# Performance work log

Measured on AMD Instinct MI355X. Metric: run time of the kernel, lower is better.

Reference implementation:

```python
import jax, jax.numpy as jnp
import numpy as np

N, T, U, D, V = 16, 512, 64, 512, 500


def _ragged_indices(enc_len, dec_len):
    """Flat (b, t, u) index triples for all valid T_i x U_i pairs, concatenated."""
    bs, ts, us = [], [], []
    for i in range(len(enc_len)):
        t, u = int(enc_len[i]), int(dec_len[i])
        tt, uu = np.meshgrid(np.arange(t), np.arange(u), indexing='ij')
        bs.append(np.full(t * u, i, dtype=np.int32))
        ts.append(tt.ravel().astype(np.int32))
        us.append(uu.ravel().astype(np.int32))
    return (jnp.asarray(np.concatenate(bs)),
            jnp.asarray(np.concatenate(ts)),
            jnp.asarray(np.concatenate(us)))


def setup_inputs() -> dict:
    key = jax.random.key(0)
    k1, k2, k3, k4 = jax.random.split(key, 4)
    encoder_out = jax.random.normal(k1, (N, T, D), dtype=jnp.float32)
    decoder_out = jax.random.normal(k2, (N, U, D), dtype=jnp.float32)
    # Concrete (non-traced) ragged lengths, as in the torch module's .tolist().
    rng = np.random.default_rng(0)
    enc_len = rng.integers(T // 2, T + 1, size=N)
    dec_len = rng.integers(U // 2, U + 1, size=N)
    b_idx, t_idx, u_idx = _ragged_indices(enc_len, dec_len)
    # nn.Linear(D, V) parameters
    bound = 1.0 / np.sqrt(D)
    W = jax.random.uniform(k3, (V, D), minval=-bound, maxval=bound, dtype=jnp.float32)
    b = jax.random.uniform(k4, (V,), minval=-bound, maxval=bound, dtype=jnp.float32)
    return {
        'encoder_out': encoder_out,
        'decoder_out': decoder_out,
        'W': W,
        'b': b,
        'b_idx': b_idx,
        't_idx': t_idx,
        'u_idx': u_idx,
    }


def reference(encoder_out, decoder_out, W, b, b_idx, t_idx, u_idx):
    # Ragged broadcast add: x[k] = encoder_out[b_k, t_k] + decoder_out[b_k, u_k]
    x = encoder_out[b_idx, t_idx] + decoder_out[b_idx, u_idx]  # (sum_TU, D)
    activations = jnp.tanh(x)
    logits = activations @ W.T + b  # (sum_TU, V)
    return logits
```

## Files before the change

kernel.cpp:

```cpp
#include <hip/hip_runtime.h>
#include <hip/hip_bf16.h>


typedef __attribute__((ext_vector_type(4))) int   i32x4;
typedef __attribute__((ext_vector_type(4))) float f32x4;
typedef __attribute__((ext_vector_type(8))) short short8;

__device__ __forceinline__ unsigned short f2bf(float v) {
    unsigned int u = __float_as_uint(v);
    u += 0x7fffu + ((u >> 16) & 1u);
    return (unsigned short)(u >> 16);
}

__device__ __forceinline__ unsigned pack_bf16x2(float a, float b) {
    __hip_bfloat162 h = __float22bfloat162_rn(make_float2(a, b));
    unsigned u;
    __builtin_memcpy(&u, &h, 4);
    return u;
}

__device__ __forceinline__ float bflo(unsigned u) { return __uint_as_float(u << 16); }
__device__ __forceinline__ float bfhi(unsigned u) { return __uint_as_float(u & 0xffff0000u); }

__device__ __forceinline__ float tanh_fast(float x) {
    float t = __builtin_amdgcn_exp2f(x * 2.8853900817779268f);
    return (t - 1.0f) * __builtin_amdgcn_rcpf(t + 1.0f);
}

__device__ __forceinline__ unsigned q8(float t) {
    return __float_as_uint(fmaf(t, 127.0f, 12582912.0f)) & 0xffu;
}

__global__ void prep_cast_kernel(const float* __restrict__ src,
                                 unsigned short* __restrict__ dst, int n4) {
    const int i = blockIdx.x * blockDim.x + threadIdx.x;
    if (i < n4) {
        const float4 v = reinterpret_cast<const float4*>(src)[i];
        uint2 p;
        p.x = pack_bf16x2(v.x, v.y);
        p.y = pack_bf16x2(v.z, v.w);
        reinterpret_cast<uint2*>(dst)[i] = p;
    }
}

__global__ void prep_wq_kernel(const float* __restrict__ W,
                               signed char* __restrict__ qW, float* __restrict__ fac) {
    const int n   = blockIdx.x;
    const int tid = threadIdx.x;
    float w = 0.0f;
    if (n < 500) w = W[n * 512 + tid];
    float m = fabsf(w);
    #pragma unroll
    for (int off = 32; off; off >>= 1) m = fmaxf(m, __shfl_xor(m, off));
    __shared__ float wm[8];
    if ((tid & 63) == 0) wm[tid >> 6] = m;
    __syncthreads();
    const float mx = fmaxf(fmaxf(fmaxf(wm[0], wm[1]), fmaxf(wm[2], wm[3])),
                           fmaxf(fmaxf(wm[4], wm[5]), fmaxf(wm[6], wm[7])));
    const float inv = (mx > 0.0f) ? 127.0f / mx : 0.0f;
    qW[n * 512 + tid] = (signed char)(int)rintf(w * inv);
    if (tid == 0) fac[n] = mx * (1.0f / (127.0f * 127.0f));
}

template<bool BF16G>
__global__ __launch_bounds__(512, 4)
void joiner_i8_kernel(const float* __restrict__ enc, const float* __restrict__ dec,
                      const unsigned short* __restrict__ encB,
                      const unsigned short* __restrict__ decB,
                      const float* __restrict__ bias,
                      const signed char* __restrict__ qW, const float* __restrict__ fac,
                      const int* __restrict__ b_idx, const int* __restrict__ t_idx,
                      const int* __restrict__ u_idx,
                      float* __restrict__ out, int M)
{
    __shared__ unsigned char Abuf[65792];

    const int tid  = threadIdx.x;
    const int lane = tid & 63;
    const int m0   = blockIdx.x * 64;

    const int rr = tid >> 7;
    int eoff_l, doff_l;
    {
        const int rc = min(m0 + ((lane & 15) << 2) + rr, M - 1);
        const int bi = b_idx[rc];
        eoff_l = ((bi << 9) + t_idx[rc]) << 9;
        doff_l = ((bi << 6) + u_idx[rc]) << 9;
    }

    {
        const int kq  = tid & 127;
        const int kq4 = kq << 2;

        if constexpr (BF16G) {
            uint2 es[6], dsv[6];
            #pragma unroll
            for (int i = 0; i < 6; ++i) {
                const int eo = __builtin_amdgcn_readlane(eoff_l, i);
                const int dofs = __builtin_amdgcn_readlane(doff_l, i);
                es[i]  = *reinterpret_cast<const uint2*>(encB + eo + kq4);
                dsv[i] = *reinterpret_cast<const uint2*>(decB + dofs + kq4);
            }
            #pragma unroll
            for (int p = 0; p < 16; ++p) {
                const int s = p % 6;
                const uint2 e = es[s];
                const uint2 d = dsv[s];
                if (p + 6 < 16) {
                    const int eo = __builtin_amdgcn_readlane(eoff_l, p + 6);
                    const int dofs = __builtin_amdgcn_readlane(doff_l, p + 6);
                    es[s]  = *reinterpret_cast<const uint2*>(encB + eo + kq4);
                    dsv[s] = *reinterpret_cast<const uint2*>(decB + dofs + kq4);
                }
                const unsigned u = q8(tanh_fast(bflo(e.x) + bflo(d.x)))
                                 | (q8(tanh_fast(bfhi(e.x) + bfhi(d.x))) << 8)
                                 | (q8(tanh_fast(bflo(e.y) + bflo(d.y))) << 16)
                                 | (q8(tanh_fast(bfhi(e.y) + bfhi(d.y))) << 24);
                const int r = p * 4 + rr;
                const int byteoff = (r * 512) + ((kq * 4) ^ ((r & 7) << 4));
                *reinterpret_cast<unsigned*>(&Abuf[byteoff]) = u;
            }
        } else {
            float4 es[6], dsv[6];
            #pragma unroll
            for (int i = 0; i < 6; ++i) {
                const int eo = __builtin_amdgcn_readlane(eoff_l, i);
                const int dofs = __builtin_amdgcn_readlane(doff_l, i);
                es[i]  = *reinterpret_cast<const float4*>(enc + eo + kq4);
                dsv[i] = *reinterpret_cast<const float4*>(dec + dofs + kq4);
            }
            #pragma unroll
            for (int p = 0; p < 16; ++p) {
                const int s = p % 6;
                const float4 e = es[s];
                const float4 d = dsv[s];
                if (p + 6 < 16) {
                    const int eo = __builtin_amdgcn_readlane(eoff_l, p + 6);
                    const int dofs = __builtin_amdgcn_readlane(doff_l, p + 6);
                    es[s]  = *reinterpret_cast<const float4*>(enc + eo + kq4);
                    dsv[s] = *reinterpret_cast<const float4*>(dec + dofs + kq4);
                }
                const unsigned u = q8(tanh_fast(e.x + d.x))
                                 | (q8(tanh_fast(e.y + d.y)) << 8)
                                 | (q8(tanh_fast(e.z + d.z)) << 16)
                                 | (q8(tanh_fast(e.w + d.w)) << 24);
                const int r = p * 4 + rr;
                const int byteoff = (r * 512) + ((kq * 4) ^ ((r & 7) << 4));
                *reinterpret_cast<unsigned*>(&Abuf[byteoff]) = u;
            }
        }
    }

    const int wv   = tid >> 6;
    const int l15  = lane & 15;
    const int lk   = lane >> 4;
    const int n_wave = wv << 6;
    const int a_swz  = (l15 & 7) << 4;

    i32x4 acc[4][4];
    #pragma unroll
    for (int mf = 0; mf < 4; ++mf)
        #pragma unroll
        for (int nf = 0; nf < 4; ++nf)
            acc[mf][nf] = (i32x4)(0);

    const signed char* wq = qW + ((size_t)(n_wave + l15)) * 512 + lk * 16;
    auto loadB = [&](int ks, int nf) -> i32x4 {
        return *reinterpret_cast<const i32x4*>(wq + nf * (16 * 512) + ks * 64);
    };

    i32x4 Bf[2][4];
    #pragma unroll
    for (int nf = 0; nf < 4; ++nf) Bf[0][nf] = loadB(0, nf);
    #pragma unroll
    for (int nf = 0; nf < 4; ++nf) Bf[1][nf] = loadB(1, nf);

    __syncthreads();

    #pragma unroll
    for (int ks = 0; ks < 8; ++ks) {
        i32x4 a[4];
        #pragma unroll
        for (int mf = 0; mf < 4; ++mf) {
            const int addr = ((mf * 16 + l15) << 9) + ((ks * 64 + lk * 16) ^ a_swz);
            a[mf] = *reinterpret_cast<const i32x4*>(&Abuf[addr]);
        }
        __builtin_amdgcn_s_setprio(1);
        #pragma unroll
        for (int mf = 0; mf < 4; ++mf)
            #pragma unroll
            for (int nf = 0; nf < 4; ++nf)
                acc[mf][nf] = __builtin_amdgcn_mfma_i32_16x16x64_i8(a[mf], Bf[ks & 1][nf], acc[mf][nf], 0, 0, 0);
        __builtin_amdgcn_s_setprio(0);
        if (ks < 6) {
            #pragma unroll
            for (int nf = 0; nf < 4; ++nf) Bf[ks & 1][nf] = loadB(ks + 2, nf);
        }
    }

    float accf[4][4][4];
    #pragma unroll
    for (int nf = 0; nf < 4; ++nf) {
        const int col = n_wave + nf * 16 + l15;
        const float fc = (col < 500) ? fac[col] : 0.0f;
        const float bv = (col < 500) ? bias[col] : 0.0f;
        #pragma unroll
        for (int mf = 0; mf < 4; ++mf)
            #pragma unroll
            for (int j = 0; j < 4; ++j)
                accf[mf][nf][j] = (float)acc[mf][nf][j] * fc + bv;
    }

    float* Obuf = reinterpret_cast<float*>(Abuf);
    #pragma unroll
    for (int h = 0; h < 2; ++h) {
        __syncthreads();
        if ((wv >> 2) == h) {
            const int lcol = (wv & 3) << 6;
            #pragma unroll
            for (int mf = 0; mf < 4; ++mf)
                #pragma unroll
                for (int nf = 0; nf < 4; ++nf)
                    #pragma unroll
                    for (int j = 0; j < 4; ++j) {
                        const int r = mf * 16 + lk * 4 + j;
                        Obuf[r * 257 + lcol + nf * 16 + l15] = accf[mf][nf][j];
                    }
        }
        __syncthreads();
        #pragma unroll
        for (int i = 0; i < 8; ++i) {
            const int linear = i * 512 + tid;
            const int r  = linear >> 6;
            const int c4 = linear & 63;
            const int row = m0 + r;
            const int col = (h << 8) + (c4 << 2);
            if (row < M && col < 500) {
                const f32x4 v = *reinterpret_cast<const f32x4*>(&Obuf[r * 257 + (c4 << 2)]);
                __builtin_nontemporal_store(v, reinterpret_cast<f32x4*>(&out[(size_t)row * 500 + col]));
            }
        }
    }
}

__global__ __launch_bounds__(512, 4)
void joiner_fallback_kernel(const float* __restrict__ enc, const float* __restrict__ dec,
                            const float* __restrict__ W, const float* __restrict__ bias,
                            const int* __restrict__ b_idx, const int* __restrict__ t_idx,
                            const int* __restrict__ u_idx,
                            float* __restrict__ out, int M)
{
    __shared__ unsigned char Abuf[65792];
    const int tid  = threadIdx.x;
    const int lane = tid & 63;
    const int m0   = blockIdx.x * 64;

    const int rr = tid >> 7;
    int eoff_l, doff_l;
    {
        const int rc = min(m0 + ((lane & 15) << 2) + rr, M - 1);
        const int bi = b_idx[rc];
        eoff_l = ((bi << 9) + t_idx[rc]) << 9;
        doff_l = ((bi << 6) + u_idx[rc]) << 9;
    }
    {
        const int kq  = tid & 127;
        const int kq4 = kq << 2;
        float4 es[6], dsv[6];
        #pragma unroll
        for (int i = 0; i < 6; ++i) {
            es[i]  = *reinterpret_cast<const float4*>(enc + __builtin_amdgcn_readlane(eoff_l, i) + kq4);
            dsv[i] = *reinterpret_cast<const float4*>(dec + __builtin_amdgcn_readlane(doff_l, i) + kq4);
        }
        #pragma unroll
        for (int p = 0; p < 16; ++p) {
            const int s = p % 6;
            const float4 e = es[s];
            const float4 d = dsv[s];
            if (p + 6 < 16) {
                es[s]  = *reinterpret_cast<const float4*>(enc + __builtin_amdgcn_readlane(eoff_l, p + 6) + kq4);
                dsv[s] = *reinterpret_cast<const float4*>(dec + __builtin_amdgcn_readlane(doff_l, p + 6) + kq4);
            }
            uint2 packed;
            packed.x = pack_bf16x2(tanh_fast(e.x + d.x), tanh_fast(e.y + d.y));
            packed.y = pack_bf16x2(tanh_fast(e.z + d.z), tanh_fast(e.w + d.w));
            const int r = p * 4 + rr;
            const int byteoff = (r * 1024 + kq * 8) ^ ((r & 7) << 4);
            *reinterpret_cast<uint2*>(&Abuf[byteoff]) = packed;
        }
    }
    const int wv   = tid >> 6;
    const int l15  = lane & 15;
    const int lk   = lane >> 4;
    const int n_wave = wv << 6;
    const int a_swz  = (l15 & 7) << 4;

    f32x4 acc[4][4];
    #pragma unroll
    for (int mf = 0; mf < 4; ++mf)
        #pragma unroll
        for (int nf = 0; nf < 4; ++nf)
            acc[mf][nf] = (f32x4)(0.0f);

    const float* wpf = W + (((size_t)(n_wave + l15)) << 9) + (lk << 3);
    const int colbase = n_wave + l15;
    auto loadB = [&](int ks, int nf) -> short8 {
        short8 b;
        float4 w0 = make_float4(0,0,0,0), w1 = make_float4(0,0,0,0);
        if (colbase + nf * 16 < 500) {
            const float4* q = reinterpret_cast<const float4*>(wpf + nf * 8192 + ks * 32);
            w0 = q[0]; w1 = q[1];
        }
        b[0] = (short)f2bf(w0.x); b[1] = (short)f2bf(w0.y);
        b[2] = (short)f2bf(w0.z); b[3] = (short)f2bf(w0.w);
        b[4] = (short)f2bf(w1.x); b[5] = (short)f2bf(w1.y);
        b[6] = (short)f2bf(w1.z); b[7] = (short)f2bf(w1.w);
        return b;
    };

    short8 Bf[2][4];
    #pragma unroll
    for (int nf = 0; nf < 4; ++nf) Bf[0][nf] = loadB(0, nf);
    #pragma unroll
    for (int nf = 0; nf < 4; ++nf) Bf[1][nf] = loadB(1, nf);
    __syncthreads();
    #pragma unroll
    for (int ks = 0; ks < 16; ++ks) {
        short8 a[4];
        #pragma unroll
        for (int mf = 0; mf < 4; ++mf) {
            const int addr = (((mf * 16 + l15) << 10) + ks * 64 + lk * 16) ^ a_swz;
            a[mf] = *reinterpret_cast<const short8*>(&Abuf[addr]);
        }
        #pragma unroll
        for (int mf = 0; mf < 4; ++mf)
            #pragma unroll
            for (int nf = 0; nf < 4; ++nf)
                acc[mf][nf] = __builtin_amdgcn_mfma_f32_16x16x32_bf16(a[mf], Bf[ks & 1][nf], acc[mf][nf], 0, 0, 0);
        if (ks < 14) {
            #pragma unroll
            for (int nf = 0; nf < 4; ++nf) Bf[ks & 1][nf] = loadB(ks + 2, nf);
        }
    }
    #pragma unroll
    for (int nf = 0; nf < 4; ++nf) {
        const int col = n_wave + nf * 16 + l15;
        const float bv = (col < 500) ? bias[col] : 0.0f;
        #pragma unroll
        for (int mf = 0; mf < 4; ++mf)
            #pragma unroll
            for (int j = 0; j < 4; ++j)
                acc[mf][nf][j] += bv;
    }
    float* Obuf = reinterpret_cast<float*>(Abuf);
    #pragma unroll
    for (int h = 0; h < 2; ++h) {
        __syncthreads();
        if ((wv >> 2) == h) {
            const int lcol = (wv & 3) << 6;
            #pragma unroll
            for (int mf = 0; mf < 4; ++mf)
                #pragma unroll
                for (int nf = 0; nf < 4; ++nf)
                    #pragma unroll
                    for (int j = 0; j < 4; ++j) {
                        const int r = mf * 16 + lk * 4 + j;
                        Obuf[r * 257 + lcol + nf * 16 + l15] = acc[mf][nf][j];
                    }
        }
        __syncthreads();
        #pragma unroll
        for (int i = 0; i < 8; ++i) {
            const int linear = i * 512 + tid;
            const int r  = linear >> 6;
            const int c4 = linear & 63;
            const int row = m0 + r;
            const int col = (h << 8) + (c4 << 2);
            if (row < M && col < 500) {
                const f32x4 v = *reinterpret_cast<const f32x4*>(&Obuf[r * 257 + (c4 << 2)]);
                __builtin_nontemporal_store(v, reinterpret_cast<f32x4*>(&out[(size_t)row * 500 + col]));
            }
        }
    }
}

extern "C" void kernel_launch(void* const* d_in, const int* in_sizes, int n_in,
                              void* d_out, int out_size, void* d_ws, size_t ws_size,
                              hipStream_t stream) {
    const float* enc  = (const float*)d_in[0];
    const float* dec  = (const float*)d_in[1];
    const float* W    = (const float*)d_in[2];
    const float* bias = (const float*)d_in[3];
    const int* bi = (const int*)d_in[4];
    const int* ti = (const int*)d_in[5];
    const int* ui = (const int*)d_in[6];
    float* out = (float*)d_out;

    const int M = in_sizes[4];
    const int grid = (M + 63) / 64;

    const int enc_n  = in_sizes[0];
    const int dec_n  = in_sizes[1];
    const size_t qw_bytes = (size_t)512 * 512;
    const size_t fac_off  = qw_bytes;
    const size_t enc_off  = fac_off + 2048;
    const size_t dec_off  = enc_off + (size_t)enc_n * 2;
    const size_t need_i8  = fac_off + 2048;
    const size_t need_all = dec_off + (size_t)dec_n * 2;

    if (ws_size >= need_all) {
        signed char* qW = (signed char*)d_ws;
        float* fac = (float*)((char*)d_ws + fac_off);
        unsigned short* encB = (unsigned short*)((char*)d_ws + enc_off);
        unsigned short* decB = (unsigned short*)((char*)d_ws + dec_off);
        prep_wq_kernel<<<512, 512, 0, stream>>>(W, qW, fac);
        prep_cast_kernel<<<(enc_n / 4 + 255) / 256, 256, 0, stream>>>(enc, encB, enc_n / 4);
        prep_cast_kernel<<<(dec_n / 4 + 255) / 256, 256, 0, stream>>>(dec, decB, dec_n / 4);
        joiner_i8_kernel<true><<<grid, 512, 0, stream>>>(
            enc, dec, encB, decB, bias, qW, fac, bi, ti, ui, out, M);
    } else if (ws_size >= need_i8) {
        signed char* qW = (signed char*)d_ws;
        float* fac = (float*)((char*)d_ws + fac_off);
        prep_wq_kernel<<<512, 512, 0, stream>>>(W, qW, fac);
        joiner_i8_kernel<false><<<grid, 512, 0, stream>>>(
            enc, dec, nullptr, nullptr, bias, qW, fac, bi, ti, ui, out, M);
    } else {
        joiner_fallback_kernel<<<grid, 512, 0, stream>>>(
            enc, dec, W, bias, bi, ti, ui, out, M);
    }
}
```

Before: 239.2 us.

## Split A-tile gather into K halves and overlap second half with MFMA

Adds a new bf16-input joiner kernel that gathers and quantizes only the first half of K into shared memory before the matmul starts. The second half's global loads are issued early and consumed inside the first half's MFMA loop, and B fragments are double-buffered from global. The aim is to hide gather and tanh latency behind tensor-core work instead of doing all of it serially up front. The cost is more registers and an extra barrier, which may reduce occupancy. The old template is reduced to its fp32 variant for the fallback path.

```diff
diff --git a/kernel.cpp b/kernel.cpp
--- a/kernel.cpp
+++ b/kernel.cpp
@@ -62,11 +62,170 @@
     if (tid == 0) fac[n] = mx * (1.0f / (127.0f * 127.0f));
 }
 
-template<bool BF16G>
+__global__ __launch_bounds__(512, 4)
+void joiner_i8p_kernel(const unsigned short* __restrict__ encB,
+                       const unsigned short* __restrict__ decB,
+                       const float* __restrict__ bias,
+                       const signed char* __restrict__ qW, const float* __restrict__ fac,
+                       const int* __restrict__ b_idx, const int* __restrict__ t_idx,
+                       const int* __restrict__ u_idx,
+                       float* __restrict__ out, int M)
+{
+    __shared__ unsigned char Abuf[65792];
+
+    const int tid  = threadIdx.x;
+    const int lane = tid & 63;
+    const int wv   = tid >> 6;
+    const int m0   = blockIdx.x * 64;
+
+    int eoff_l, doff_l;
+    {
+        const int rc = min(m0 + ((lane & 7) << 3) + wv, M - 1);
+        const int bi = b_idx[rc];
+        eoff_l = ((bi << 9) + t_idx[rc]) << 9;
+        doff_l = ((bi << 6) + u_idx[rc]) << 9;
+    }
+
+    auto gload = [&](int p, int h, uint2& e, uint2& d) {
+        const int eo   = __builtin_amdgcn_readlane(eoff_l, p) + h * 256 + lane * 4;
+        const int dofs = __builtin_amdgcn_readlane(doff_l, p) + h * 256 + lane * 4;
+        e = *reinterpret_cast<const uint2*>(encB + eo);
+        d = *reinterpret_cast<const uint2*>(decB + dofs);
+    };
+    auto gconsume = [&](int p, int h, uint2 e, uint2 d) {
+        const unsigned u = q8(tanh_fast(bflo(e.x) + bflo(d.x)))
+                         | (q8(tanh_fast(bfhi(e.x) + bfhi(d.x))) << 8)
+                         | (q8(tanh_fast(bflo(e.y) + bflo(d.y))) << 16)
+                         | (q8(tanh_fast(bfhi(e.y) + bfhi(d.y))) << 24);
+        const int r = p * 8 + wv;
+        const int byteoff = h * 16384 + r * 256 + ((lane * 4) ^ ((r & 7) << 4));
+        *reinterpret_cast<unsigned*>(&Abuf[byteoff]) = u;
+    };
+
+    const int l15  = lane & 15;
+    const int lk   = lane >> 4;
+    const int n_wave = wv << 6;
+    const int a_swz  = (l15 & 7) << 4;
+
+    const signed char* wq = qW + ((size_t)(n_wave + l15)) * 512 + lk * 16;
+    auto loadB = [&](int ks, int nf) -> i32x4 {
+        return *reinterpret_cast<const i32x4*>(wq + nf * (16 * 512) + ks * 64);
+    };
+
+    uint2 ge[8], gd[8];
+    #pragma unroll
+    for (int p = 0; p < 8; ++p) gload(p, 0, ge[p], gd[p]);
+    #pragma unroll
+    for (int p = 0; p < 8; ++p) gconsume(p, 0, ge[p], gd[p]);
+    #pragma unroll
+    for (int p = 0; p < 8; ++p) gload(p, 1, ge[p], gd[p]);
+
+    i32x4 acc[4][4];
+    #pragma unroll
+    for (int mf = 0; mf < 4; ++mf)
+        #pragma unroll
+        for (int nf = 0; nf < 4; ++nf)
+            acc[mf][nf] = (i32x4)(0);
+
+    i32x4 Bf[2][4];
+    #pragma unroll
+    for (int nf = 0; nf < 4; ++nf) Bf[0][nf] = loadB(0, nf);
+    #pragma unroll
+    for (int nf = 0; nf < 4; ++nf) Bf[1][nf] = loadB(1, nf);
+
+    __syncthreads();
+
+    #pragma unroll
+    for (int ks = 0; ks < 4; ++ks) {
+        gconsume(2 * ks,     1, ge[2 * ks],     gd[2 * ks]);
+        gconsume(2 * ks + 1, 1, ge[2 * ks + 1], gd[2 * ks + 1]);
+        i32x4 a[4];
+        #pragma unroll
+        for (int mf = 0; mf < 4; ++mf) {
+            const int addr = (mf * 16 + l15) * 256 + ((ks * 64 + lk * 16) ^ a_swz);
+            a[mf] = *reinterpret_cast<const i32x4*>(&Abuf[addr]);
+        }
+        __builtin_amdgcn_s_setprio(1);
+        #pragma unroll
+        for (int mf = 0; mf < 4; ++mf)
+            #pragma unroll
+            for (int nf = 0; nf < 4; ++nf)
+                acc[mf][nf] = __builtin_amdgcn_mfma_i32_16x16x64_i8(a[mf], Bf[ks & 1][nf], acc[mf][nf], 0, 0, 0);
+        __builtin_amdgcn_s_setprio(0);
+        #pragma unroll
+        for (int nf = 0; nf < 4; ++nf) Bf[ks & 1][nf] = loadB(ks + 2, nf);
+    }
+
+    __syncthreads();
+
+    #pragma unroll
+    for (int ks = 4; ks < 8; ++ks) {
+        i32x4 a[4];
+        #pragma unroll
+        for (int mf = 0; mf < 4; ++mf) {
+            const int addr = 16384 + (mf * 16 + l15) * 256 + (((ks - 4) * 64 + lk * 16) ^ a_swz);
+            a[mf] = *reinterpret_cast<const i32x4*>(&Abuf[addr]);
+        }
+        __builtin_amdgcn_s_setprio(1);
+        #pragma unroll
+        for (int mf = 0; mf < 4; ++mf)
+            #pragma unroll
+            for (int nf = 0; nf < 4; ++nf)
+                acc[mf][nf] = __builtin_amdgcn_mfma_i32_16x16x64_i8(a[mf], Bf[ks & 1][nf], acc[mf][nf], 0, 0, 0);
+        __builtin_amdgcn_s_setprio(0);
+        if (ks < 6) {
+            #pragma unroll
+            for (int nf = 0; nf < 4; ++nf) Bf[ks & 1][nf] = loadB(ks + 2, nf);
+        }
+    }
+
+    float accf[4][4][4];
+    #pragma unroll
+    for (int nf = 0; nf < 4; ++nf) {
+        const int col = n_wave + nf * 16 + l15;
+        const float fc = (col < 500) ? fac[col] : 0.0f;
+        const float bv = (col < 500) ? bias[col] : 0.0f;
+        #pragma unroll
+        for (int mf = 0; mf < 4; ++mf)
+            #pragma unroll
+            for (int j = 0; j < 4; ++j)
+                accf[mf][nf][j] = (float)acc[mf][nf][j] * fc + bv;
+    }
+
+    float* Obuf = reinterpret_cast<float*>(Abuf);
+    #pragma unroll
+    for (int h = 0; h < 2; ++h) {
+        __syncthreads();
+        if ((wv >> 2) == h) {
+            const int lcol = (wv & 3) << 6;
+            #pragma unroll
+            for (int mf = 0; mf < 4; ++mf)
+                #pragma unroll
+                for (int nf = 0; nf < 4; ++nf)
+                    #pragma unroll
+                    for (int j = 0; j < 4; ++j) {
+                        const int r = mf * 16 + lk * 4 + j;
+                        Obuf[r * 257 + lcol + nf * 16 + l15] = accf[mf][nf][j];
+                    }
+        }
+        __syncthreads();
+        #pragma unroll
+        for (int i = 0; i < 8; ++i) {
+            const int linear = i * 512 + tid;
+            const int r  = linear >> 6;
+            const int c4 = linear & 63;
+            const int row = m0 + r;
+            const int col = (h << 8) + (c4 << 2);
+            if (row < M && col < 500) {
+                const f32x4 v = *reinterpret_cast<const f32x4*>(&Obuf[r * 257 + (c4 << 2)]);
+                __builtin_nontemporal_store(v, reinterpret_cast<f32x4*>(&out[(size_t)row * 500 + col]));
+            }
+        }
+    }
+}
+
 __global__ __launch_bounds__(512, 4)
 void joiner_i8_kernel(const float* __restrict__ enc, const float* __restrict__ dec,
-                      const unsigned short* __restrict__ encB,
-                      const unsigned short* __restrict__ decB,
                       const float* __restrict__ bias,
                       const signed char* __restrict__ qW, const float* __restrict__ fac,
                       const int* __restrict__ b_idx, const int* __restrict__ t_idx,
@@ -74,7 +233,6 @@
                       float* __restrict__ out, int M)
 {
     __shared__ unsigned char Abuf[65792];
-
     const int tid  = threadIdx.x;
     const int lane = tid & 63;
     const int m0   = blockIdx.x * 64;
@@ -87,70 +245,33 @@
         eoff_l = ((bi << 9) + t_idx[rc]) << 9;
         doff_l = ((bi << 6) + u_idx[rc]) << 9;
     }
-
     {
         const int kq  = tid & 127;
         const int kq4 = kq << 2;
-
-        if constexpr (BF16G) {
-            uint2 es[6], dsv[6];
-            #pragma unroll
-            for (int i = 0; i < 6; ++i) {
-                const int eo = __builtin_amdgcn_readlane(eoff_l, i);
-                const int dofs = __builtin_amdgcn_readlane(doff_l, i);
-                es[i]  = *reinterpret_cast<const uint2*>(encB + eo + kq4);
-                dsv[i] = *reinterpret_cast<const uint2*>(decB + dofs + kq4);
+        float4 es[6], dsv[6];
+        #pragma unroll
+        for (int i = 0; i < 6; ++i) {
+            es[i]  = *reinterpret_cast<const float4*>(enc + __builtin_amdgcn_readlane(eoff_l, i) + kq4);
+            dsv[i] = *reinterpret_cast<const float4*>(dec + __builtin_amdgcn_readlane(doff_l, i) + kq4);
+        }
+        #pragma unroll
+        for (int p = 0; p < 16; ++p) {
+            const int s = p % 6;
+            const float4 e = es[s];
+            const float4 d = dsv[s];
+            if (p + 6 < 16) {
+                es[s]  = *reinterpret_cast<const float4*>(enc + __builtin_amdgcn_readlane(eoff_l, p + 6) + kq4);
+                dsv[s] = *reinterpret_cast<const float4*>(dec + __builtin_amdgcn_readlane(doff_l, p + 6) + kq4);
             }
-            #pragma unroll
-            for (int p = 0; p < 16; ++p) {
-                const int s = p % 6;
-                const uint2 e = es[s];
-                const uint2 d = dsv[s];
-                if (p + 6 < 16) {
-                    const int eo = __builtin_amdgcn_readlane(eoff_l, p + 6);
-                    const int dofs = __builtin_amdgcn_readlane(doff_l, p + 6);
-                    es[s]  = *reinterpret_cast<const uint2*>(encB + eo + kq4);
-                    dsv[s] = *reinterpret_cast<const uint2*>(decB + dofs + kq4);
-                }
-                const unsigned u = q8(tanh_fast(bflo(e.x) + bflo(d.x)))
-                                 | (q8(tanh_fast(bfhi(e.x) + bfhi(d.x))) << 8)
-                                 | (q8(tanh_fast(bflo(e.y) + bflo(d.y))) << 16)
-                                 | (q8(tanh_fast(bfhi(e.y) + bfhi(d.y))) << 24);
-                const int r = p * 4 + rr;
-                const int byteoff = (r * 512) + ((kq * 4) ^ ((r & 7) << 4));
-                *reinterpret_cast<unsigned*>(&Abuf[byteoff]) = u;
-            }
-        } else {
-            float4 es[6], dsv[6];
-            #pragma unroll
-            for (int i = 0; i < 6; ++i) {
-                const int eo = __builtin_amdgcn_readlane(eoff_l, i);
-                const int dofs = __builtin_amdgcn_readlane(doff_l, i);
-                es[i]  = *reinterpret_cast<const float4*>(enc + eo + kq4);
-                dsv[i] = *reinterpret_cast<const float4*>(dec + dofs + kq4);
-            }
-            #pragma unroll
-            for (int p = 0; p < 16; ++p) {
-                const int s = p % 6;
-                const float4 e = es[s];
-                const float4 d = dsv[s];
-                if (p + 6 < 16) {
-                    const int eo = __builtin_amdgcn_readlane(eoff_l, p + 6);
-                    const int dofs = __builtin_amdgcn_readlane(doff_l, p + 6);
-                    es[s]  = *reinterpret_cast<const float4*>(enc + eo + kq4);
-                    dsv[s] = *reinterpret_cast<const float4*>(dec + dofs + kq4);
-                }
-                const unsigned u = q8(tanh_fast(e.x + d.x))
-                                 | (q8(tanh_fast(e.y + d.y)) << 8)
-                                 | (q8(tanh_fast(e.z + d.z)) << 16)
-                                 | (q8(tanh_fast(e.w + d.w)) << 24);
-                const int r = p * 4 + rr;
-                const int byteoff = (r * 512) + ((kq * 4) ^ ((r & 7) << 4));
-                *reinterpret_cast<unsigned*>(&Abuf[byteoff]) = u;
-            }
-        }
-    }
-
+            const unsigned u = q8(tanh_fast(e.x + d.x))
+                             | (q8(tanh_fast(e.y + d.y)) << 8)
+                             | (q8(tanh_fast(e.z + d.z)) << 16)
+                             | (q8(tanh_fast(e.w + d.w)) << 24);
+            const int r = p * 4 + rr;
+            const int byteoff = (r * 512) + ((kq * 4) ^ ((r & 7) << 4));
+            *reinterpret_cast<unsigned*>(&Abuf[byteoff]) = u;
+        }
+    }
     const int wv   = tid >> 6;
     const int l15  = lane & 15;
     const int lk   = lane >> 4;
@@ -416,14 +537,14 @@
         prep_wq_kernel<<<512, 512, 0, stream>>>(W, qW, fac);
         prep_cast_kernel<<<(enc_n / 4 + 255) / 256, 256, 0, stream>>>(enc, encB, enc_n / 4);
         prep_cast_kernel<<<(dec_n / 4 + 255) / 256, 256, 0, stream>>>(dec, decB, dec_n / 4);
-        joiner_i8_kernel<true><<<grid, 512, 0, stream>>>(
-            enc, dec, encB, decB, bias, qW, fac, bi, ti, ui, out, M);
+        joiner_i8p_kernel<<<grid, 512, 0, stream>>>(
+            encB, decB, bias, qW, fac, bi, ti, ui, out, M);
     } else if (ws_size >= need_i8) {
         signed char* qW = (signed char*)d_ws;
         float* fac = (float*)((char*)d_ws + fac_off);
         prep_wq_kernel<<<512, 512, 0, stream>>>(W, qW, fac);
-        joiner_i8_kernel<false><<<grid, 512, 0, stream>>>(
-            enc, dec, nullptr, nullptr, bias, qW, fac, bi, ti, ui, out, M);
+        joiner_i8_kernel<<<grid, 512, 0, stream>>>(
+            enc, dec, bias, qW, fac, bi, ti, ui, out, M);
     } else {
         joiner_fallback_kernel<<<grid, 512, 0, stream>>>(
             enc, dec, W, bias, bi, ti, ui, out, M);
```

Result: slower. 332.1 us (+38.8%).
